# Kernel optimization log

Hardware: AMD Instinct MI355X
Metric: run time of the kernel (lower is better)

The kernel has to match this reference:

```python
import jax, jax.numpy as jnp
import numpy as np

NUM_LAYERS = 4
N_HEADS = 16
D_MODEL = 1024
D_FF = 4096
K = 7
L = 2048
C_IN = 4
C_OUT = 4
HD = D_MODEL // N_HEADS  # 64
EPS = 1e-5
THETA = 10000.0


def setup_inputs() -> dict:
    key = jax.random.key(0)
    ks = iter(jax.random.split(key, 32))

    def rn(shape, scale=0.02):
        return jax.random.normal(next(ks), shape, jnp.float32) * scale

    return {
        "x": jax.random.normal(next(ks), (C_IN, L), jnp.float32),
        "conv_in_w": rn((D_MODEL, C_IN, K)),
        "conv_in_b": rn((D_MODEL,)),
        "ln1_w": jnp.ones((NUM_LAYERS, D_MODEL), jnp.float32),
        "ln1_b": jnp.zeros((NUM_LAYERS, D_MODEL), jnp.float32),
        "wq": rn((NUM_LAYERS, D_MODEL, D_MODEL)),
        "wk": rn((NUM_LAYERS, D_MODEL, D_MODEL)),
        "wv": rn((NUM_LAYERS, D_MODEL, D_MODEL)),
        "wo": rn((NUM_LAYERS, D_MODEL, D_MODEL)),
        "ln2_w": jnp.ones((NUM_LAYERS, D_MODEL), jnp.float32),
        "ln2_b": jnp.zeros((NUM_LAYERS, D_MODEL), jnp.float32),
        "w1": rn((NUM_LAYERS, D_FF, D_MODEL)),
        "b1": rn((NUM_LAYERS, D_FF)),
        "w2": rn((NUM_LAYERS, D_FF, D_FF)),
        "b2": rn((NUM_LAYERS, D_FF)),
        "w3": rn((NUM_LAYERS, D_MODEL, D_FF)),
        "b3": rn((NUM_LAYERS, D_MODEL)),
        "conv_out_w": rn((C_OUT, D_MODEL, K)),
        "conv_out_b": rn((C_OUT,)),
    }


def conv1d_causal(x, w, b):
    # x: [C_in, L]; w: [C_out, C_in, K]; causal left-pad (K-1, 0)
    xp = jnp.pad(x, ((0, 0), (K - 1, 0)))[None]  # [1, C_in, L+K-1]
    y = jax.lax.conv_general_dilated(xp, w, (1,), "VALID", dimension_numbers=("NCH", "OIH", "NCH"))[0]
    return y + b[:, None]


def rms_norm(x, w, b):
    # eqx.nn.RMSNorm with weight and bias, applied per token
    inv = jax.lax.rsqrt(jnp.mean(x * x, axis=-1, keepdims=True) + EPS)
    return x * inv * w + b


def rope(x):
    # x: [L, H, HD]; eqx RotaryPositionalEmbedding (rotate-half / NeoX style)
    seq = x.shape[0]
    freqs = 1.0 / (THETA ** (jnp.arange(0, HD, 2, dtype=jnp.float32) / HD))  # [HD/2]
    ang = jnp.arange(seq, dtype=jnp.float32)[:, None] * freqs[None, :]  # [L, HD/2]
    cos = jnp.tile(jnp.cos(ang), (1, 2))[:, None, :]  # [L, 1, HD]
    sin = jnp.tile(jnp.sin(ang), (1, 2))[:, None, :]
    x1, x2 = jnp.split(x, 2, axis=-1)
    rot = jnp.concatenate((-x2, x1), axis=-1)
    return x * cos + rot * sin


def block(x, ln1_w, ln1_b, wq, wk, wv, wo, ln2_w, ln2_b, w1, b1, w2, b2, w3, b3):
    seq = x.shape[0]
    h = rms_norm(x, ln1_w, ln1_b)
    q = (h @ wq.T).reshape(seq, N_HEADS, HD)
    k = (h @ wk.T).reshape(seq, N_HEADS, HD)
    v = (h @ wv.T).reshape(seq, N_HEADS, HD)
    q = rope(q)
    k = rope(k)
    scores = jnp.einsum("shd,Shd->hsS", q / jnp.sqrt(jnp.float32(HD)), k)  # [H, L, L]
    causal = jnp.tril(jnp.ones((seq, seq), bool))
    scores = jnp.where(causal[None], scores, jnp.finfo(scores.dtype).min)
    attn = jax.nn.softmax(scores, axis=-1)
    o = jnp.einsum("hsS,Shd->shd", attn, v).reshape(seq, D_MODEL)
    x = x + o @ wo.T
    # eqx.nn.MLP depth=2: Linear->relu->Linear->relu->Linear
    h = rms_norm(x, ln2_w, ln2_b)
    h = jax.nn.relu(h @ w1.T + b1)
    h = jax.nn.relu(h @ w2.T + b2)
    return x + h @ w3.T + b3


def _forward(x, conv_in_w, conv_in_b, ln1_w, ln1_b, wq, wk, wv, wo, ln2_w, ln2_b, w1, b1, w2, b2, w3, b3, conv_out_w, conv_out_b):
    h = jax.nn.relu(conv1d_causal(x, conv_in_w, conv_in_b))  # [D_MODEL, L]
    h = h.T  # [L, D_MODEL]
    for i in range(NUM_LAYERS):
        h = block(h, ln1_w[i], ln1_b[i], wq[i], wk[i], wv[i], wo[i], ln2_w[i], ln2_b[i], w1[i], b1[i], w2[i], b2[i], w3[i], b3[i])
    h = h.T  # [D_MODEL, L]
    return conv1d_causal(h, conv_out_w, conv_out_b)  # [C_OUT, L]


def reference(x, conv_in_w, conv_in_b, ln1_w, ln1_b, wq, wk, wv, wo, ln2_w, ln2_b, w1, b1, w2, b2, w3, b3, conv_out_w, conv_out_b):
    return _forward(x, conv_in_w, conv_in_b, ln1_w, ln1_b, wq, wk, wv, wo, ln2_w, ln2_b, w1, b1, w2, b2, w3, b3, conv_out_w, conv_out_b)
```

## Files before the change

kernel.cpp:

```cpp
#include <hip/hip_runtime.h>
#include <math.h>

#define L_SEQ 2048
#define DM 1024
#define DFF 4096
#define NH 16
#define HD 64

typedef __bf16 bf16_t;
typedef __bf16 bf16x4 __attribute__((ext_vector_type(4)));
typedef __bf16 bf16x8 __attribute__((ext_vector_type(8)));
typedef float floatx4 __attribute__((ext_vector_type(4)));

__device__ __forceinline__ void gl_lds16(const void* g, void* l) {
    __builtin_amdgcn_global_load_lds((const __attribute__((address_space(1))) void*)g,
                                     (__attribute__((address_space(3))) void*)l, 16, 0, 0);
}

__global__ __launch_bounds__(256) void conv_in_kernel(const float* __restrict__ x,
                                                      const float* __restrict__ w,
                                                      const float* __restrict__ b,
                                                      float* __restrict__ h) {
    int gid = blockIdx.x * 256 + threadIdx.x;
    int d = gid & (DM - 1);
    int l = gid >> 10;
    float acc = b[d];
    const float* wd = w + d * 28;
#pragma unroll
    for (int c = 0; c < 4; ++c) {
#pragma unroll
        for (int k = 0; k < 7; ++k) {
            int t = l + k - 6;
            float xv = (t >= 0) ? x[c * L_SEQ + t] : 0.f;
            acc = fmaf(xv, wd[c * 7 + k], acc);
        }
    }
    h[(size_t)l * DM + d] = fmaxf(acc, 0.f);
}

__global__ __launch_bounds__(256) void rmsnorm_kernel(const float* __restrict__ h,
                                                      const float* __restrict__ w,
                                                      const float* __restrict__ b,
                                                      bf16_t* __restrict__ out) {
    int l = blockIdx.x;
    int t = threadIdx.x;
    const float* row = h + (size_t)l * DM;
    float4 xv = *(const float4*)(row + t * 4);
    float ss = xv.x * xv.x + xv.y * xv.y + xv.z * xv.z + xv.w * xv.w;
#pragma unroll
    for (int off = 1; off < 64; off <<= 1) ss += __shfl_xor(ss, off, 64);
    __shared__ float red[4];
    if ((t & 63) == 0) red[t >> 6] = ss;
    __syncthreads();
    float tot = red[0] + red[1] + red[2] + red[3];
    float inv = rsqrtf(tot * (1.f / DM) + 1e-5f);
    float4 wv = *(const float4*)(w + t * 4);
    float4 bv = *(const float4*)(b + t * 4);
    bf16x4 ov;
    ov.x = (bf16_t)fmaf(xv.x * inv, wv.x, bv.x);
    ov.y = (bf16_t)fmaf(xv.y * inv, wv.y, bv.y);
    ov.z = (bf16_t)fmaf(xv.z * inv, wv.z, bv.z);
    ov.w = (bf16_t)fmaf(xv.w * inv, wv.w, bv.w);
    *(bf16x4*)(out + (size_t)l * DM + t * 4) = ov;
}

__global__ __launch_bounds__(256) void cvt_bf16(const float* __restrict__ in,
                                                bf16_t* __restrict__ out, int n4) {
    int i = blockIdx.x * 256 + threadIdx.x;
    if (i < n4) {
        float4 v = *(const float4*)(in + (size_t)i * 4);
        bf16x4 o = {(bf16_t)v.x, (bf16_t)v.y, (bf16_t)v.z, (bf16_t)v.w};
        *(bf16x4*)(out + (size_t)i * 4) = o;
    }
}

__global__ __launch_bounds__(256) void cvt_qkvw(const float* __restrict__ wq,
                                                const float* __restrict__ wk,
                                                const float* __restrict__ wv,
                                                bf16_t* __restrict__ out) {
    int i = blockIdx.x * 256 + threadIdx.x;
    int layer = i / 786432;
    int rem = i - layer * 786432;
    int sel = rem / 262144;
    int idx = rem - sel * 262144;
    const float* src = (sel == 0 ? wq : sel == 1 ? wk : wv) + (size_t)layer * 1048576 + (size_t)idx * 4;
    float4 v = *(const float4*)src;
    bf16x4 o = {(bf16_t)v.x, (bf16_t)v.y, (bf16_t)v.z, (bf16_t)v.w};
    *(bf16x4*)(out + (size_t)i * 4) = o;
}

template <int TN, bool BIAS, bool RELU, bool RES, bool OUTBF>
__global__ __launch_bounds__(256) void gemm_bt(const bf16_t* __restrict__ A,
                                               const bf16_t* __restrict__ B,
                                               const float* __restrict__ bias,
                                               const float* __restrict__ res,
                                               void* __restrict__ Cout,
                                               int M, int N, int K) {
    constexpr int WMI = (TN == 128) ? 4 : 2;
    __shared__ alignas(16) bf16_t As[128 * 32];
    __shared__ alignas(16) bf16_t Bs[TN * 32];

    const int t = threadIdx.x;
    const int wave = t >> 6;
    const int lane = t & 63;
    const int quad = lane >> 4;
    const int l16 = lane & 15;
    const int m0 = blockIdx.y * 128;
    const int n0 = blockIdx.x * TN;

    const int wm = (TN == 128) ? (wave & 1) * 64 : wave * 32;
    const int wn = (TN == 128) ? (wave >> 1) * 64 : 0;

    floatx4 acc[WMI][4];
#pragma unroll
    for (int i = 0; i < WMI; ++i)
#pragma unroll
        for (int j = 0; j < 4; ++j) acc[i][j] = (floatx4)0.f;

    const int ldrow = t >> 2;
    const int ldk = (t & 3) * 8;
    const bf16_t* ga = A + (size_t)(m0 + ldrow) * K + ldk;
    const bf16_t* gb = B + (size_t)(n0 + ldrow) * K + ldk;
    char* lA = (char*)As + (size_t)wave * 1024;
    char* lB = (char*)Bs + (size_t)wave * 1024;

    for (int k0 = 0; k0 < K; k0 += 32) {
        gl_lds16(ga, lA);
        gl_lds16(ga + (size_t)64 * K, lA + 4096);
        gl_lds16(gb, lB);
        if (TN == 128) gl_lds16(gb + (size_t)64 * K, lB + 4096);
        ga += 32;
        gb += 32;
        __syncthreads();

        bf16x8 af[WMI], bfr[4];
#pragma unroll
        for (int i = 0; i < WMI; ++i)
            af[i] = *(const bf16x8*)((const char*)As + (size_t)(wm + i * 16 + l16) * 64 + quad * 16);
#pragma unroll
        for (int j = 0; j < 4; ++j)
            bfr[j] = *(const bf16x8*)((const char*)Bs + (size_t)(wn + j * 16 + l16) * 64 + quad * 16);
#pragma unroll
        for (int i = 0; i < WMI; ++i)
#pragma unroll
            for (int j = 0; j < 4; ++j)
                acc[i][j] = __builtin_amdgcn_mfma_f32_16x16x32_bf16(af[i], bfr[j], acc[i][j], 0, 0, 0);
        __syncthreads();
    }

#pragma unroll
    for (int i = 0; i < WMI; ++i) {
        const int m = m0 + wm + i * 16 + quad * 4;
#pragma unroll
        for (int j = 0; j < 4; ++j) {
            const int n = n0 + wn + j * 16 + l16;
            float bv = 0.f;
            if (BIAS) bv = bias[n];
#pragma unroll
            for (int r = 0; r < 4; ++r) {
                float v = acc[i][j][r] + bv;
                if (RELU) v = fmaxf(v, 0.f);
                if (RES) v += res[(size_t)(m + r) * N + n];
                if (OUTBF) ((bf16_t*)Cout)[(size_t)(m + r) * N + n] = (bf16_t)v;
                else ((float*)Cout)[(size_t)(m + r) * N + n] = v;
            }
        }
    }
}

__global__ __launch_bounds__(256) void rope_kernel(bf16_t* __restrict__ qkv) {
    int gid = blockIdx.x * 256 + threadIdx.x;
    int j = gid & 31;
    int hh = (gid >> 5) & 15;
    int l = gid >> 9;
    float freq = powf(10000.f, -(float)(2 * j) * (1.f / 64.f));
    float ang = (float)l * freq;
    float s = sinf(ang), c = cosf(ang);
    size_t base = (size_t)l * 3072 + hh * HD + j;
    float q1 = (float)qkv[base], q2 = (float)qkv[base + 32];
    qkv[base] = (bf16_t)(q1 * c - q2 * s);
    qkv[base + 32] = (bf16_t)(q2 * c + q1 * s);
    size_t kb = base + 1024;
    float k1 = (float)qkv[kb], k2 = (float)qkv[kb + 32];
    qkv[kb] = (bf16_t)(k1 * c - k2 * s);
    qkv[kb + 32] = (bf16_t)(k2 * c + k1 * s);
}

__global__ __launch_bounds__(256) void v_transpose(const bf16_t* __restrict__ qkvb,
                                                   bf16_t* __restrict__ vt) {
    __shared__ bf16_t Ts[64 * 72];
    const int h = blockIdx.x;
    const int tt = blockIdx.y;
    const int t = threadIdx.x;
#pragma unroll
    for (int i = 0; i < 2; ++i) {
        int idx = t + i * 256;
        int row = idx >> 3, dg = idx & 7;
        *(bf16x8*)(Ts + row * 72 + dg * 8) =
            *(const bf16x8*)(qkvb + (size_t)(tt * 64 + row) * 3072 + 2048 + h * 64 + dg * 8);
    }
    __syncthreads();
#pragma unroll
    for (int i = 0; i < 2; ++i) {
        int idx = t + i * 256;
        int d = idx >> 3, tg = idx & 7;
        bf16x8 v;
#pragma unroll
        for (int s = 0; s < 8; ++s) v[s] = Ts[(tg * 8 + s) * 72 + d];
        *(bf16x8*)(vt + ((size_t)h * 64 + d) * 2048 + tt * 64 + tg * 8) = v;
    }
}

__global__ __launch_bounds__(256) void attn_mfma(const bf16_t* __restrict__ qkvb,
                                                 const bf16_t* __restrict__ vt,
                                                 bf16_t* __restrict__ o) {
    __shared__ alignas(16) bf16_t Qs[64 * 72];
    __shared__ alignas(16) bf16_t Ks[64 * 72];
    __shared__ alignas(16) bf16_t Vs[64 * 72];
    __shared__ alignas(16) bf16_t Ps[4][16 * 72];
    const int t = threadIdx.x;
    const int wave = t >> 6;
    const int lane = t & 63;
    const int quad = lane >> 4;
    const int l16 = lane & 15;
    const int h = blockIdx.x;
    const int y = blockIdx.y;
    const int qt = (y < 16) ? (31 - y) : (y - 16);
    const int l0 = qt * 64;

#pragma unroll
    for (int i = 0; i < 2; ++i) {
        int idx = t + i * 256;
        int row = idx >> 3, dg = idx & 7;
        *(bf16x8*)(Qs + row * 72 + dg * 8) =
            *(const bf16x8*)(qkvb + (size_t)(l0 + row) * 3072 + h * HD + dg * 8);
    }

    float m_r[4], l_r[4];
    floatx4 acc_o[4];
#pragma unroll
    for (int r = 0; r < 4; ++r) { m_r[r] = -1e30f; l_r[r] = 0.f; }
#pragma unroll
    for (int n = 0; n < 4; ++n) acc_o[n] = (floatx4)0.f;

    for (int jt = 0; jt <= qt; ++jt) {
        const int j0 = jt * 64;
        __syncthreads();
#pragma unroll
        for (int i = 0; i < 2; ++i) {
            int idx = t + i * 256;
            int row = idx >> 3, dg = idx & 7;
            *(bf16x8*)(Ks + row * 72 + dg * 8) =
                *(const bf16x8*)(qkvb + (size_t)(j0 + row) * 3072 + 1024 + h * HD + dg * 8);
            *(bf16x8*)(Vs + row * 72 + dg * 8) =
                *(const bf16x8*)(vt + ((size_t)h * HD + row) * 2048 + j0 + dg * 8);
        }
        __syncthreads();

        bf16x8 aq0 = *(const bf16x8*)(Qs + (wave * 16 + l16) * 72 + quad * 8);
        bf16x8 aq1 = *(const bf16x8*)(Qs + (wave * 16 + l16) * 72 + 32 + quad * 8);
        floatx4 sacc[4];
#pragma unroll
        for (int j = 0; j < 4; ++j) {
            bf16x8 bk0 = *(const bf16x8*)(Ks + (j * 16 + l16) * 72 + quad * 8);
            bf16x8 bk1 = *(const bf16x8*)(Ks + (j * 16 + l16) * 72 + 32 + quad * 8);
            floatx4 s = (floatx4)0.f;
            s = __builtin_amdgcn_mfma_f32_16x16x32_bf16(aq0, bk0, s, 0, 0, 0);
            s = __builtin_amdgcn_mfma_f32_16x16x32_bf16(aq1, bk1, s, 0, 0, 0);
            sacc[j] = s;
        }

        const bool diag = (jt == qt);
        float mt[4];
#pragma unroll
        for (int r = 0; r < 4; ++r) mt[r] = -1e30f;
#pragma unroll
        for (int j = 0; j < 4; ++j)
#pragma unroll
            for (int r = 0; r < 4; ++r) {
                float sv = sacc[j][r] * 0.125f;
                if (diag && (j * 16 + l16) > (wave * 16 + quad * 4 + r)) sv = -1e30f;
                sacc[j][r] = sv;
                mt[r] = fmaxf(mt[r], sv);
            }
#pragma unroll
        for (int r = 0; r < 4; ++r) {
            mt[r] = fmaxf(mt[r], __shfl_xor(mt[r], 1, 64));
            mt[r] = fmaxf(mt[r], __shfl_xor(mt[r], 2, 64));
            mt[r] = fmaxf(mt[r], __shfl_xor(mt[r], 4, 64));
            mt[r] = fmaxf(mt[r], __shfl_xor(mt[r], 8, 64));
        }
        float alpha[4], rs[4];
#pragma unroll
        for (int r = 0; r < 4; ++r) {
            float mn = fmaxf(m_r[r], mt[r]);
            alpha[r] = __expf(m_r[r] - mn);
            m_r[r] = mn;
            rs[r] = 0.f;
        }
#pragma unroll
        for (int j = 0; j < 4; ++j)
#pragma unroll
            for (int r = 0; r < 4; ++r) {
                float p = __expf(sacc[j][r] - m_r[r]);
                sacc[j][r] = p;
                rs[r] += p;
            }
#pragma unroll
        for (int r = 0; r < 4; ++r) {
            rs[r] += __shfl_xor(rs[r], 1, 64);
            rs[r] += __shfl_xor(rs[r], 2, 64);
            rs[r] += __shfl_xor(rs[r], 4, 64);
            rs[r] += __shfl_xor(rs[r], 8, 64);
            l_r[r] = l_r[r] * alpha[r] + rs[r];
        }
#pragma unroll
        for (int n = 0; n < 4; ++n)
#pragma unroll
            for (int r = 0; r < 4; ++r) acc_o[n][r] *= alpha[r];

        bf16_t* pw = Ps[wave];
#pragma unroll
        for (int j = 0; j < 4; ++j)
#pragma unroll
            for (int r = 0; r < 4; ++r)
                pw[(quad * 4 + r) * 72 + j * 16 + l16] = (bf16_t)sacc[j][r];

        bf16x8 ap0 = *(const bf16x8*)(pw + l16 * 72 + quad * 8);
        bf16x8 ap1 = *(const bf16x8*)(pw + l16 * 72 + 32 + quad * 8);
#pragma unroll
        for (int n = 0; n < 4; ++n) {
            bf16x8 bv0 = *(const bf16x8*)(Vs + (n * 16 + l16) * 72 + quad * 8);
            bf16x8 bv1 = *(const bf16x8*)(Vs + (n * 16 + l16) * 72 + 32 + quad * 8);
            acc_o[n] = __builtin_amdgcn_mfma_f32_16x16x32_bf16(ap0, bv0, acc_o[n], 0, 0, 0);
            acc_o[n] = __builtin_amdgcn_mfma_f32_16x16x32_bf16(ap1, bv1, acc_o[n], 0, 0, 0);
        }
    }

#pragma unroll
    for (int r = 0; r < 4; ++r) {
        float inv = 1.f / l_r[r];
        int row = l0 + wave * 16 + quad * 4 + r;
#pragma unroll
        for (int n = 0; n < 4; ++n)
            o[(size_t)row * DM + h * HD + n * 16 + l16] = (bf16_t)(acc_o[n][r] * inv);
    }
}

__global__ __launch_bounds__(256) void conv_out_kernel(const float* __restrict__ h,
                                                       const float* __restrict__ w,
                                                       const float* __restrict__ b,
                                                       float* __restrict__ out) {
    int c = blockIdx.x >> 11;
    int l = blockIdx.x & 2047;
    int t = threadIdx.x;
    float acc = 0.f;
    const float* wc = w + c * (DM * 7);
    for (int idx = t; idx < DM * 7; idx += 256) {
        int d = idx / 7;
        int kk = idx - d * 7;
        int tt = l + kk - 6;
        if (tt >= 0) acc = fmaf(h[(size_t)tt * DM + d], wc[idx], acc);
    }
#pragma unroll
    for (int off = 1; off < 64; off <<= 1) acc += __shfl_xor(acc, off, 64);
    __shared__ float red[4];
    if ((t & 63) == 0) red[t >> 6] = acc;
    __syncthreads();
    if (t == 0) out[blockIdx.x] = red[0] + red[1] + red[2] + red[3] + b[c];
}

extern "C" void kernel_launch(void* const* d_in, const int* in_sizes, int n_in,
                              void* d_out, int out_size, void* d_ws, size_t ws_size,
                              hipStream_t stream) {
    const float* x = (const float*)d_in[0];
    const float* conv_in_w = (const float*)d_in[1];
    const float* conv_in_b = (const float*)d_in[2];
    const float* ln1_w = (const float*)d_in[3];
    const float* ln1_b = (const float*)d_in[4];
    const float* wq = (const float*)d_in[5];
    const float* wk = (const float*)d_in[6];
    const float* wv = (const float*)d_in[7];
    const float* wo = (const float*)d_in[8];
    const float* ln2_w = (const float*)d_in[9];
    const float* ln2_b = (const float*)d_in[10];
    const float* w1 = (const float*)d_in[11];
    const float* b1 = (const float*)d_in[12];
    const float* w2 = (const float*)d_in[13];
    const float* b2 = (const float*)d_in[14];
    const float* w3 = (const float*)d_in[15];
    const float* b3 = (const float*)d_in[16];
    const float* conv_out_w = (const float*)d_in[17];
    const float* conv_out_b = (const float*)d_in[18];

    char* W = (char*)d_ws;
    float* h = (float*)(W);
    bf16_t* qkvb = (bf16_t*)(W + (8ull << 20));
    bf16_t* hn = (bf16_t*)(W + (20ull << 20));
    bf16_t* ob = (bf16_t*)(W + (24ull << 20));
    bf16_t* f1 = (bf16_t*)(W + (28ull << 20));
    bf16_t* f2 = (bf16_t*)(W + (44ull << 20));
    bf16_t* vtb = (bf16_t*)(W + (60ull << 20));
    bf16_t* qkvw = (bf16_t*)(W + (64ull << 20));
    bf16_t* wob = (bf16_t*)(W + (88ull << 20));
    bf16_t* w1b = (bf16_t*)(W + (96ull << 20));
    bf16_t* w2b = (bf16_t*)(W + (128ull << 20));
    bf16_t* w3b = (bf16_t*)(W + (256ull << 20));

    cvt_qkvw<<<12288, 256, 0, stream>>>(wq, wk, wv, qkvw);
    cvt_bf16<<<4096, 256, 0, stream>>>(wo, wob, 1048576);
    cvt_bf16<<<16384, 256, 0, stream>>>(w1, w1b, 4194304);
    cvt_bf16<<<65536, 256, 0, stream>>>(w2, w2b, 16777216);
    cvt_bf16<<<16384, 256, 0, stream>>>(w3, w3b, 4194304);

    conv_in_kernel<<<(L_SEQ * DM) / 256, 256, 0, stream>>>(x, conv_in_w, conv_in_b, h);

    for (int layer = 0; layer < 4; ++layer) {
        const float* ln1w = ln1_w + layer * DM;
        const float* ln1b = ln1_b + layer * DM;
        const float* ln2w = ln2_w + layer * DM;
        const float* ln2b = ln2_b + layer * DM;
        const bf16_t* qkvw_l = qkvw + (size_t)layer * 3072 * 1024;
        const bf16_t* wob_l = wob + (size_t)layer * DM * DM;
        const bf16_t* w1b_l = w1b + (size_t)layer * DFF * DM;
        const bf16_t* w2b_l = w2b + (size_t)layer * DFF * DFF;
        const bf16_t* w3b_l = w3b + (size_t)layer * DM * DFF;
        const float* b1_l = b1 + (size_t)layer * DFF;
        const float* b2_l = b2 + (size_t)layer * DFF;
        const float* b3_l = b3 + (size_t)layer * DM;

        rmsnorm_kernel<<<L_SEQ, 256, 0, stream>>>(h, ln1w, ln1b, hn);
        gemm_bt<128, false, false, false, true><<<dim3(3072 / 128, L_SEQ / 128), 256, 0, stream>>>(
            hn, qkvw_l, nullptr, nullptr, qkvb, L_SEQ, 3072, 1024);
        rope_kernel<<<(L_SEQ * NH * 32) / 256, 256, 0, stream>>>(qkvb);
        v_transpose<<<dim3(NH, L_SEQ / 64), 256, 0, stream>>>(qkvb, vtb);
        attn_mfma<<<dim3(NH, L_SEQ / 64), 256, 0, stream>>>(qkvb, vtb, ob);
        gemm_bt<64, false, false, true, false><<<dim3(DM / 64, L_SEQ / 128), 256, 0, stream>>>(
            ob, wob_l, nullptr, h, h, L_SEQ, DM, DM);
        rmsnorm_kernel<<<L_SEQ, 256, 0, stream>>>(h, ln2w, ln2b, hn);
        gemm_bt<128, true, true, false, true><<<dim3(DFF / 128, L_SEQ / 128), 256, 0, stream>>>(
            hn, w1b_l, b1_l, nullptr, f1, L_SEQ, DFF, 1024);
        gemm_bt<128, true, true, false, true><<<dim3(DFF / 128, L_SEQ / 128), 256, 0, stream>>>(
            f1, w2b_l, b2_l, nullptr, f2, L_SEQ, DFF, DFF);
        gemm_bt<64, true, false, true, false><<<dim3(DM / 64, L_SEQ / 128), 256, 0, stream>>>(
            f2, w3b_l, b3_l, h, h, L_SEQ, DM, DFF);
    }

    conv_out_kernel<<<4 * L_SEQ, 256, 0, stream>>>(h, conv_out_w, conv_out_b, (float*)d_out);
}
```

Baseline: 2.177 ms.

## Add 512-thread 128x256-tile pipelined GEMM for QKV and MLP up projections

```diff
diff --git a/kernel.cpp b/kernel.cpp
--- a/kernel.cpp
+++ b/kernel.cpp
@@ -163,6 +163,106 @@
                 if (RES) v += res[(size_t)(m + r) * N + n];
                 if (OUTBF) ((bf16_t*)Cout)[(size_t)(m + r) * N + n] = (bf16_t)v;
                 else ((float*)Cout)[(size_t)(m + r) * N + n] = v;
+            }
+        }
+    }
+}
+
+template <bool BIASRELU>
+__global__ __launch_bounds__(512, 1) void gemm_pl(const bf16_t* __restrict__ A,
+                                                  const bf16_t* __restrict__ B,
+                                                  const float* __restrict__ bias,
+                                                  bf16_t* __restrict__ C,
+                                                  int M, int N, int K) {
+    __shared__ alignas(16) char smem[49152];
+    const int t = threadIdx.x;
+    const int w = t >> 6;
+    const int lane = t & 63;
+    const int quad = lane >> 4;
+    const int l16 = lane & 15;
+    const int bm = blockIdx.y * 128;
+    const int bn = blockIdx.x * 256;
+    const int wm = (w >> 2) * 64;
+    const int wn = (w & 3) * 64;
+
+    const int swz = (quad ^ ((l16 >> 1) & 3)) << 4;
+    int aoff[4], boff[4];
+#pragma unroll
+    for (int i = 0; i < 4; ++i) {
+        aoff[i] = (wm + i * 16 + l16) * 64 + swz;
+        boff[i] = 8192 + (wn + i * 16 + l16) * 64 + swz;
+    }
+
+    const int srow = w * 16 + (lane >> 2);
+    const int scl = (((lane & 3) ^ ((lane >> 3) & 3)) << 4);
+    const char* pA = (const char*)(A + (size_t)(bm + srow) * K) + scl;
+    const char* pB = (const char*)(B + (size_t)(bn + srow) * K) + scl;
+    const size_t r128 = (size_t)K * 256;
+    const int ldw = w * 1024;
+
+    const int NT = K >> 5;
+
+    floatx4 acc[4][4];
+#pragma unroll
+    for (int i = 0; i < 4; ++i)
+#pragma unroll
+        for (int j = 0; j < 4; ++j) acc[i][j] = (floatx4)0.f;
+
+#pragma unroll
+    for (int tt = 0; tt < 2; ++tt) {
+        char* lb = smem + tt * 24576;
+        gl_lds16(pA + (size_t)tt * 64, lb + ldw);
+        gl_lds16(pB + (size_t)tt * 64, lb + 8192 + ldw);
+        gl_lds16(pB + (size_t)tt * 64 + r128, lb + 8192 + ldw + 8192);
+    }
+    asm volatile("s_waitcnt vmcnt(3)" ::: "memory");
+    __builtin_amdgcn_s_barrier();
+
+    for (int tile = 0; tile < NT; ++tile) {
+        char* cb = smem + (tile & 1) * 24576;
+        const bool st = (tile + 2) < NT;
+        const size_t gof = (size_t)(tile + 2) * 64;
+
+        bf16x8 af[4], bfr[4];
+#pragma unroll
+        for (int i = 0; i < 4; ++i) af[i] = *(const bf16x8*)(cb + aoff[i]);
+#pragma unroll
+        for (int j = 0; j < 4; ++j) bfr[j] = *(const bf16x8*)(cb + boff[j]);
+        asm volatile("s_waitcnt lgkmcnt(0)" ::: "memory");
+        __builtin_amdgcn_sched_barrier(0);
+        __builtin_amdgcn_s_barrier();
+
+        if (st) {
+            gl_lds16(pA + gof, cb + ldw);
+            gl_lds16(pB + gof, cb + 8192 + ldw);
+            gl_lds16(pB + gof + r128, cb + 8192 + ldw + 8192);
+        }
+
+        __builtin_amdgcn_s_setprio(1);
+#pragma unroll
+        for (int i = 0; i < 4; ++i)
+#pragma unroll
+            for (int j = 0; j < 4; ++j)
+                acc[i][j] = __builtin_amdgcn_mfma_f32_16x16x32_bf16(af[i], bfr[j], acc[i][j], 0, 0, 0);
+        __builtin_amdgcn_s_setprio(0);
+
+        if (st) asm volatile("s_waitcnt vmcnt(3)" ::: "memory");
+        else    asm volatile("s_waitcnt vmcnt(0)" ::: "memory");
+        __builtin_amdgcn_s_barrier();
+    }
+
+#pragma unroll
+    for (int j = 0; j < 4; ++j) {
+        const int n = bn + wn + j * 16 + l16;
+        const float bv = BIASRELU ? bias[n] : 0.f;
+#pragma unroll
+        for (int i = 0; i < 4; ++i) {
+            const int m = bm + wm + i * 16 + quad * 4;
+#pragma unroll
+            for (int r = 0; r < 4; ++r) {
+                float v = acc[i][j][r] + bv;
+                if (BIASRELU) v = fmaxf(v, 0.f);
+                C[(size_t)(m + r) * N + n] = (bf16_t)v;
             }
         }
     }
@@ -430,18 +530,18 @@
         const float* b3_l = b3 + (size_t)layer * DM;
 
         rmsnorm_kernel<<<L_SEQ, 256, 0, stream>>>(h, ln1w, ln1b, hn);
-        gemm_bt<128, false, false, false, true><<<dim3(3072 / 128, L_SEQ / 128), 256, 0, stream>>>(
-            hn, qkvw_l, nullptr, nullptr, qkvb, L_SEQ, 3072, 1024);
+        gemm_pl<false><<<dim3(3072 / 256, L_SEQ / 128), 512, 0, stream>>>(
+            hn, qkvw_l, nullptr, qkvb, L_SEQ, 3072, 1024);
         rope_kernel<<<(L_SEQ * NH * 32) / 256, 256, 0, stream>>>(qkvb);
         v_transpose<<<dim3(NH, L_SEQ / 64), 256, 0, stream>>>(qkvb, vtb);
         attn_mfma<<<dim3(NH, L_SEQ / 64), 256, 0, stream>>>(qkvb, vtb, ob);
         gemm_bt<64, false, false, true, false><<<dim3(DM / 64, L_SEQ / 128), 256, 0, stream>>>(
             ob, wob_l, nullptr, h, h, L_SEQ, DM, DM);
         rmsnorm_kernel<<<L_SEQ, 256, 0, stream>>>(h, ln2w, ln2b, hn);
-        gemm_bt<128, true, true, false, true><<<dim3(DFF / 128, L_SEQ / 128), 256, 0, stream>>>(
-            hn, w1b_l, b1_l, nullptr, f1, L_SEQ, DFF, 1024);
-        gemm_bt<128, true, true, false, true><<<dim3(DFF / 128, L_SEQ / 128), 256, 0, stream>>>(
-            f1, w2b_l, b2_l, nullptr, f2, L_SEQ, DFF, DFF);
+        gemm_pl<true><<<dim3(DFF / 256, L_SEQ / 128), 512, 0, stream>>>(
+            hn, w1b_l, b1_l, f1, L_SEQ, DFF, 1024);
+        gemm_pl<true><<<dim3(DFF / 256, L_SEQ / 128), 512, 0, stream>>>(
+            f1, w2b_l, b2_l, f2, L_SEQ, DFF, DFF);
         gemm_bt<64, true, false, true, false><<<dim3(DM / 64, L_SEQ / 128), 256, 0, stream>>>(
             f2, w3b_l, b3_l, h, h, L_SEQ, DM, DFF);
     }
```

New measurement: 1.999 ms. 8.2% less time.
